# Performance work log

Hardware: AMD Instinct MI355X
Metric: run time of the kernel (lower is better)

## Reference

```python
import math
import jax, jax.numpy as jnp
import numpy as np

D_MODEL = 512
MAX_SEQ = 512
NUM_OUT = 16
H = 1  # num_heads


def _pos_encoding(d_model, seq_len):
    # sinusoidal PE, then flipped along the sequence axis (ReversedPositionalEncoding)
    pos = jnp.arange(seq_len, dtype=jnp.float32)[:, None]
    i = jnp.arange(0, d_model, 2, dtype=jnp.float32)
    ang = pos * jnp.exp(i * (-(math.log(10000.0) / d_model)))  # [S, d/2]
    pe = jnp.stack([jnp.sin(ang), jnp.cos(ang)], axis=-1).reshape(seq_len, d_model)
    return pe[::-1]


def _layernorm(x, w, b, eps=1e-5):
    m = jnp.mean(x, axis=-1, keepdims=True)
    v = jnp.mean(jnp.square(x - m), axis=-1, keepdims=True)
    return (x - m) / jnp.sqrt(v + eps) * w + b


def setup_inputs() -> dict:
    key = jax.random.key(0)
    ks = jax.random.split(key, 8)
    B = 128
    latents = jax.random.normal(ks[0], (B, D_MODEL, MAX_SEQ), dtype=jnp.float32)
    query_mask = jnp.ones((B, NUM_OUT), dtype=jnp.float32)
    query = 0.02 * jax.random.normal(ks[1], (NUM_OUT, D_MODEL), dtype=jnp.float32)
    return {
        "latents": latents,
        "query_mask": query_mask,
        "query": query,
        "ln_lat_w": jnp.ones((D_MODEL,), jnp.float32),
        "ln_lat_b": jnp.zeros((D_MODEL,), jnp.float32),
        "ln_q_w": jnp.ones((D_MODEL,), jnp.float32),
        "ln_q_b": jnp.zeros((D_MODEL,), jnp.float32),
        "Wq": 0.02 * jax.random.normal(ks[2], (D_MODEL, D_MODEL), jnp.float32),
        "bq": jnp.zeros((D_MODEL,), jnp.float32),
        "Wk": 0.02 * jax.random.normal(ks[3], (D_MODEL, D_MODEL), jnp.float32),
        "bk": jnp.zeros((D_MODEL,), jnp.float32),
        "Wv": 0.02 * jax.random.normal(ks[4], (D_MODEL, D_MODEL), jnp.float32),
        "bv": jnp.zeros((D_MODEL,), jnp.float32),
        "Wo": 0.02 * jax.random.normal(ks[5], (1, D_MODEL), jnp.float32),
        "bo": jnp.zeros((1,), jnp.float32),
    }


def reference(latents, query_mask, query, ln_lat_w, ln_lat_b, ln_q_w, ln_q_b,
              Wq, bq, Wk, bk, Wv, bv, Wo, bo):
    B, _, N = latents.shape  # latents: [B, d_model, N]
    scale = math.sqrt(D_MODEL)
    Dh = D_MODEL // H

    # cross-attention mask: query_mask [B,Nq] x all-ones latent mask [B,N]
    mask = jnp.einsum('bq,bk->bqk', query_mask, jnp.ones((B, N), latents.dtype))

    x = jnp.swapaxes(latents, 1, 2) * scale           # [B, N, d]
    x = x + _pos_encoding(D_MODEL, MAX_SEQ)[-N:]      # reversed PE, last N positions
    # dropout is identity in eval mode
    x = _layernorm(x, ln_lat_w, ln_lat_b)

    q = _layernorm(query * scale, ln_q_w, ln_q_b)     # [Nq, d]
    q = jnp.broadcast_to(q[None], (B, NUM_OUT, D_MODEL))

    qh = (q @ Wq.T + bq).reshape(B, NUM_OUT, H, Dh)
    kh = (x @ Wk.T + bk).reshape(B, N, H, Dh)
    vh = (x @ Wv.T + bv).reshape(B, N, H, Dh)

    scores = jnp.einsum('bqhd,bkhd->bhqk', qh, kh) / math.sqrt(Dh)
    scores = jnp.where(mask[:, None] == 0, -1e9, scores)
    attn_weights = jax.nn.softmax(scores, axis=-1)    # [B, H, Nq, N]

    attn = jnp.einsum('bhqk,bkhd->bqhd', attn_weights, vh).reshape(B, NUM_OUT, H * Dh)
    wipe = jnp.all(mask == 0, axis=2, keepdims=True)  # [B, Nq, 1]
    attn = jnp.where(wipe, 0.0, attn)

    logits = attn @ Wo.T + bo                         # [B, Nq, 1]
    return logits, attn_weights
```

## Files before the change

kernel.cpp:

```cpp
#include <hip/hip_runtime.h>
#include <math.h>

#define DM 512
#define NQ 16
#define NG (NQ + 1)
#define NR (NG + 2)

typedef __attribute__((ext_vector_type(2))) float f32x2;

__device__ __forceinline__ float wave_reduce_sum(float v) {
    #pragma unroll
    for (int off = 32; off > 0; off >>= 1) v += __shfl_xor(v, off, 64);
    return v;
}
__device__ __forceinline__ float wave_reduce_max(float v) {
    #pragma unroll
    for (int off = 32; off > 0; off >>= 1) v = fmaxf(v, __shfl_xor(v, off, 64));
    return v;
}

__global__ void k1_setup(const float* __restrict__ Wk, const float* __restrict__ Wv,
                         const float* __restrict__ query,
                         const float* __restrict__ ln_q_w, const float* __restrict__ ln_q_b,
                         float* __restrict__ PET, float* __restrict__ WkT,
                         float* __restrict__ WvT, float* __restrict__ q_ln, int N) {
    __shared__ float tile[64][65];
    int bx = blockIdx.x;
    int lane = threadIdx.x & 63;
    int w = threadIdx.x >> 6;

    if (bx < 128) {
        int ntile = bx & 7, jg = bx >> 3;
        int n = ntile * 64 + lane;
        float p = (float)(N - 1 - n);
        const float c = -logf(10000.f) / (float)DM;
        int jbase = jg * 16 + w * 4;
        #pragma unroll
        for (int u = 0; u < 4; ++u) {
            int j = jbase + u;
            float wj = expf((float)(2 * j) * c);
            float ang = p * wj;
            PET[(size_t)(2 * j) * N + n] = sinf(ang);
            PET[(size_t)(2 * j + 1) * N + n] = cosf(ang);
        }
    } else if (bx < 256) {
        int t = bx - 128;
        const float* W = (t >> 6) ? Wv : Wk;
        float* WT = (t >> 6) ? WvT : WkT;
        int tl = t & 63;
        int te = tl >> 3, td = tl & 7;
        #pragma unroll
        for (int i = 0; i < 16; ++i) {
            int el = w * 16 + i;
            tile[el][lane] = W[(size_t)(te * 64 + el) * DM + td * 64 + lane];
        }
        __syncthreads();
        #pragma unroll
        for (int i = 0; i < 16; ++i) {
            int dl = w * 16 + i;
            WT[(size_t)(td * 64 + dl) * DM + te * 64 + lane] = tile[lane][dl];
        }
    } else {
        const float scale = 22.627416997969522f;
        for (int qi = 0; qi < 4; ++qi) {
            int q = w * 4 + qi;
            float vals[8], s = 0.f, s2 = 0.f;
            #pragma unroll
            for (int i = 0; i < 8; ++i) {
                float x = query[q * DM + i * 64 + lane] * scale;
                vals[i] = x; s += x; s2 += x * x;
            }
            s = wave_reduce_sum(s); s2 = wave_reduce_sum(s2);
            float m = s * (1.f / DM);
            float var = s2 * (1.f / DM) - m * m;
            float rstd = rsqrtf(var + 1e-5f);
            #pragma unroll
            for (int i = 0; i < 8; ++i) {
                int d = i * 64 + lane;
                q_ln[q * DM + d] = (vals[i] - m) * rstd * ln_q_w[d] + ln_q_b[d];
            }
        }
    }
}

__global__ void k2_qh(const float* __restrict__ q_ln, const float* __restrict__ Wq,
                      const float* __restrict__ bq, float* __restrict__ qh) {
    int idx = blockIdx.x * 4 + (threadIdx.x >> 6);
    int lane = threadIdx.x & 63;
    int q = idx >> 9, e = idx & 511;
    const float4* wr = (const float4*)(Wq + (size_t)e * DM);
    const float4* xr = (const float4*)(q_ln + (size_t)q * DM);
    float4 w0 = wr[lane * 2], w1 = wr[lane * 2 + 1];
    float4 x0 = xr[lane * 2], x1 = xr[lane * 2 + 1];
    float s = w0.x * x0.x + w0.y * x0.y + w0.z * x0.z + w0.w * x0.w
            + w1.x * x1.x + w1.y * x1.y + w1.z * x1.z + w1.w * x1.w;
    s = wave_reduce_sum(s);
    if (lane == 0) qh[q * DM + e] = s + bq[e];
}

__global__ void k3_qt(const float* __restrict__ qh, const float* __restrict__ WkT,
                      const float* __restrict__ Wo, const float* __restrict__ WvT,
                      const float* __restrict__ lnw,
                      float* __restrict__ qt, float* __restrict__ A,
                      f32x2* __restrict__ A2, float* __restrict__ wvout) {
    int idx = blockIdx.x * 4 + (threadIdx.x >> 6);
    int lane = threadIdx.x & 63;
    int g = idx >> 9, d = idx & 511;
    const float4* wr;
    const float4* xr;
    if (g < NQ) {
        wr = (const float4*)(WkT + (size_t)d * DM);
        xr = (const float4*)(qh + (size_t)g * DM);
    } else {
        wr = (const float4*)(WvT + (size_t)d * DM);
        xr = (const float4*)Wo;
    }
    float4 w0 = wr[lane * 2], w1 = wr[lane * 2 + 1];
    float4 x0 = xr[lane * 2], x1 = xr[lane * 2 + 1];
    float s = w0.x * x0.x + w0.y * x0.y + w0.z * x0.z + w0.w * x0.w
            + w1.x * x1.x + w1.y * x1.y + w1.z * x1.z + w1.w * x1.w;
    s = wave_reduce_sum(s);
    if (lane == 0) {
        if (g < NQ) qt[g * DM + d] = s;
        else wvout[d] = s;
        float a = s * lnw[d];
        A[g * DM + d] = a;
        f32x2 ap; ap.x = a; ap.y = a;
        A2[g * DM + d] = ap;
    }
}

__global__ void k_consts(const float* __restrict__ A, const float* __restrict__ qt,
                         const float* __restrict__ qh, const float* __restrict__ wv,
                         const float* __restrict__ lnb, const float* __restrict__ bk,
                         const float* __restrict__ Wo, const float* __restrict__ bv,
                         float* __restrict__ consts) {
    int lane = threadIdx.x & 63;
    int w = threadIdx.x >> 6;
    int t = blockIdx.x * 4 + w;
    if (t > NQ) return;
    if (t < NQ) {
        float sa = 0.f, sc = 0.f, qb = 0.f;
        #pragma unroll
        for (int i = 0; i < 8; ++i) {
            int d = i * 64 + lane;
            sa += A[t * DM + d];
            sc = fmaf(qt[t * DM + d], lnb[d], sc);
            qb = fmaf(qh[t * DM + d], bk[d], qb);
        }
        sa = wave_reduce_sum(sa);
        sc = wave_reduce_sum(sc);
        qb = wave_reduce_sum(qb);
        if (lane == 0) { consts[t] = sa; consts[16 + t] = sc + qb; }
    } else {
        float sa = 0.f, cv = 0.f, bvo = 0.f;
        #pragma unroll
        for (int i = 0; i < 8; ++i) {
            int d = i * 64 + lane;
            sa += A[NQ * DM + d];
            cv = fmaf(wv[d], lnb[d], cv);
            bvo = fmaf(Wo[d], bv[d], bvo);
        }
        sa = wave_reduce_sum(sa);
        cv = wave_reduce_sum(cv);
        bvo = wave_reduce_sum(bvo);
        if (lane == 0) { consts[32] = sa; consts[33] = cv + bvo; }
    }
}

__launch_bounds__(256, 4)
__global__ void main2_kernel(const float* __restrict__ latents,
                             const float* __restrict__ PET,
                             const f32x2* __restrict__ A2,
                             float* __restrict__ pbuf, int N) {
    int ntiles = N >> 7;
    int ntile = blockIdx.x % ntiles;
    int dh = blockIdx.x / ntiles;
    int b = blockIdx.y;
    int lane = threadIdx.x & 63;
    int w = threadIdx.x >> 6;
    int n0 = ntile * 128 + lane * 2;

    int d0 = __builtin_amdgcn_readfirstlane(dh * 256 + w * 64);
    const float* latf = latents + (size_t)b * DM * N + (size_t)d0 * N + n0;
    const float* petf = PET + (size_t)d0 * N + n0;
    const float scale = 22.627416997969522f;
    f32x2 sc2; sc2.x = scale; sc2.y = scale;

    f32x2 acc[NG];
    #pragma unroll
    for (int i = 0; i < NG; ++i) { acc[i].x = 0.f; acc[i].y = 0.f; }
    f32x2 S1 = {0.f, 0.f}, S2 = {0.f, 0.f};

    const int U = 4;
    const int NC = 64 / U;
    f32x2 xb[2][U], pb[2][U];
    #pragma unroll
    for (int u = 0; u < U; ++u) {
        xb[0][u] = __builtin_nontemporal_load((const f32x2*)(latf + (size_t)u * N));
        pb[0][u] = *(const f32x2*)(petf + (size_t)u * N);
    }
    for (int c = 0; c < NC; c += 2) {
        #pragma unroll
        for (int u = 0; u < U; ++u) {
            size_t dd = (size_t)((c + 1) * U + u) * N;
            xb[1][u] = __builtin_nontemporal_load((const f32x2*)(latf + dd));
            pb[1][u] = *(const f32x2*)(petf + dd);
        }
        #pragma unroll
        for (int u = 0; u < U; ++u) {
            f32x2 y = xb[0][u] * sc2 + pb[0][u];
            S1 += y; S2 += y * y;
            int d = d0 + c * U + u;
            #pragma unroll
            for (int q = 0; q < NG; ++q)
                acc[q] += A2[(size_t)q * DM + d] * y;
        }
        if (c + 2 < NC) {
            #pragma unroll
            for (int u = 0; u < U; ++u) {
                size_t dd = (size_t)((c + 2) * U + u) * N;
                xb[0][u] = __builtin_nontemporal_load((const f32x2*)(latf + dd));
                pb[0][u] = *(const f32x2*)(petf + dd);
            }
        }
        #pragma unroll
        for (int u = 0; u < U; ++u) {
            f32x2 y = xb[1][u] * sc2 + pb[1][u];
            S1 += y; S2 += y * y;
            int d = d0 + (c + 1) * U + u;
            #pragma unroll
            for (int q = 0; q < NG; ++q)
                acc[q] += A2[(size_t)q * DM + d] * y;
        }
    }

    __shared__ f32x2 red[4][NR][64];
    red[w][0][lane] = S1;
    red[w][1][lane] = S2;
    #pragma unroll
    for (int i = 0; i < NG; ++i) red[w][2 + i][lane] = acc[i];
    __syncthreads();
    if (w != 0) return;

    float* pout = pbuf + (((size_t)dh * gridDim.y + b) * NR) * N + n0;
    #pragma unroll
    for (int i = 0; i < NR; ++i) {
        f32x2 t = red[0][i][lane] + red[1][i][lane] + red[2][i][lane] + red[3][i][lane];
        *(f32x2*)(pout + (size_t)i * N) = t;
    }
}

__global__ void finalize_kernel(const float* __restrict__ pbuf,
                                const float* __restrict__ consts,
                                float* __restrict__ scores,
                                float* __restrict__ vbuf, int N, int B) {
    int t = blockIdx.x * 256 + threadIdx.x;
    int ppb = N >> 1;
    int b = t / ppb;
    int n0 = (t - b * ppb) * 2;
    if (b >= B) return;

    const float* p0 = pbuf + (((size_t)0 * B + b) * NR) * N + n0;
    const float* p1 = pbuf + (((size_t)1 * B + b) * NR) * N + n0;
    f32x2 tot[NR];
    #pragma unroll
    for (int i = 0; i < NR; ++i)
        tot[i] = *(const f32x2*)(p0 + (size_t)i * N) + *(const f32x2*)(p1 + (size_t)i * N);

    f32x2 m = tot[0] * (1.f / DM);
    f32x2 ex2 = tot[1] * (1.f / DM);
    f32x2 rstd;
    rstd.x = rsqrtf(ex2.x - m.x * m.x + 1e-5f);
    rstd.y = rsqrtf(ex2.y - m.y * m.y + 1e-5f);

    float sumAv = consts[32], CvT = consts[33];
    f32x2 v = rstd * (tot[2 + NQ] - m * sumAv) + CvT;
    *(f32x2*)(vbuf + (size_t)b * N + n0) = v;

    const float isd = 0.044194173824159216f;
    #pragma unroll
    for (int q = 0; q < NQ; ++q) {
        f32x2 sc = (rstd * (tot[2 + q] - m * consts[q]) + consts[16 + q]) * isd;
        *(f32x2*)(scores + ((size_t)b * NQ + q) * N + n0) = sc;
    }
}

__global__ void softmax_kernel(const float* __restrict__ scores,
                               const float* __restrict__ vbuf,
                               const float* __restrict__ query_mask,
                               const float* __restrict__ bo,
                               float* __restrict__ out_logits,
                               float* __restrict__ out_attn, int N) {
    int r = blockIdx.x * 4 + (threadIdx.x >> 6);
    int b = r >> 4;
    int lane = threadIdx.x & 63;
    float4* attn_row = (float4*)(out_attn + (size_t)r * N);
    float qm = query_mask[r];
    int nv = N / 4;
    if (qm == 0.f) {
        float u = 1.f / (float)N;
        float4 uv = make_float4(u, u, u, u);
        for (int i = lane; i < nv; i += 64) attn_row[i] = uv;
        if (lane == 0) out_logits[r] = bo[0];
        return;
    }
    const float4* srow = (const float4*)(scores + (size_t)r * N);
    float4 sv[2];
    sv[0] = srow[lane]; sv[1] = srow[64 + lane];
    float mx = fmaxf(fmaxf(fmaxf(sv[0].x, sv[0].y), fmaxf(sv[0].z, sv[0].w)),
                     fmaxf(fmaxf(sv[1].x, sv[1].y), fmaxf(sv[1].z, sv[1].w)));
    mx = wave_reduce_max(mx);
    float sum = 0.f;
    #pragma unroll
    for (int i = 0; i < 2; ++i) {
        sv[i].x = expf(sv[i].x - mx); sv[i].y = expf(sv[i].y - mx);
        sv[i].z = expf(sv[i].z - mx); sv[i].w = expf(sv[i].w - mx);
        sum += sv[i].x + sv[i].y + sv[i].z + sv[i].w;
    }
    sum = wave_reduce_sum(sum);
    float inv = 1.f / sum;
    const float4* vrow = (const float4*)(vbuf + (size_t)b * N);
    float lp = 0.f;
    #pragma unroll
    for (int i = 0; i < 2; ++i) {
        float4 vv = vrow[i * 64 + lane];
        float4 wgt;
        wgt.x = sv[i].x * inv; wgt.y = sv[i].y * inv;
        wgt.z = sv[i].z * inv; wgt.w = sv[i].w * inv;
        attn_row[i * 64 + lane] = wgt;
        lp += wgt.x * vv.x + wgt.y * vv.y + wgt.z * vv.z + wgt.w * vv.w;
    }
    lp = wave_reduce_sum(lp);
    if (lane == 0) out_logits[r] = lp + bo[0];
}

extern "C" void kernel_launch(void* const* d_in, const int* in_sizes, int n_in,
                              void* d_out, int out_size, void* d_ws, size_t ws_size,
                              hipStream_t stream) {
    const float* latents    = (const float*)d_in[0];
    const float* query_mask = (const float*)d_in[1];
    const float* query      = (const float*)d_in[2];
    const float* ln_lat_w   = (const float*)d_in[3];
    const float* ln_lat_b   = (const float*)d_in[4];
    const float* ln_q_w     = (const float*)d_in[5];
    const float* ln_q_b     = (const float*)d_in[6];
    const float* Wq         = (const float*)d_in[7];
    const float* bq         = (const float*)d_in[8];
    const float* Wk         = (const float*)d_in[9];
    const float* bk         = (const float*)d_in[10];
    const float* Wv         = (const float*)d_in[11];
    const float* bv         = (const float*)d_in[12];
    const float* Wo         = (const float*)d_in[13];
    const float* bo         = (const float*)d_in[14];

    int B = in_sizes[1] / NQ;
    int N = in_sizes[0] / (DM * B);

    float* ws = (float*)d_ws;
    size_t off = 0;
    float* PET    = ws + off; off += (size_t)DM * N;
    float* WkT    = ws + off; off += (size_t)DM * DM;
    float* WvT    = ws + off; off += (size_t)DM * DM;
    float* q_ln   = ws + off; off += NQ * DM;
    float* qh     = ws + off; off += NQ * DM;
    float* qt     = ws + off; off += NQ * DM;
    float* A      = ws + off; off += NG * DM;
    float* A2     = ws + off; off += (size_t)NG * DM * 2;
    float* wv     = ws + off; off += DM;
    float* consts = ws + off; off += 64;
    float* scores = ws + off; off += (size_t)B * NQ * N;
    float* vbuf   = ws + off; off += (size_t)B * N;
    float* pbuf   = ws + off; off += (size_t)2 * B * NR * N;

    float* out_logits = (float*)d_out;
    float* out_attn   = out_logits + (size_t)B * NQ;

    k1_setup<<<257, 256, 0, stream>>>(Wk, Wv, query, ln_q_w, ln_q_b,
                                      PET, WkT, WvT, q_ln, N);
    k2_qh<<<NQ * DM / 4, 256, 0, stream>>>(q_ln, Wq, bq, qh);
    k3_qt<<<NG * DM / 4, 256, 0, stream>>>(qh, WkT, Wo, WvT, ln_lat_w,
                                           qt, A, (f32x2*)A2, wv);
    k_consts<<<5, 256, 0, stream>>>(A, qt, qh, wv, ln_lat_b, bk, Wo, bv, consts);
    dim3 gmain((N >> 7) * 2, B);
    main2_kernel<<<gmain, 256, 0, stream>>>(latents, PET, (const f32x2*)A2,
                                            pbuf, N);
    int fin_threads = B * (N / 2);
    finalize_kernel<<<(fin_threads + 255) / 256, 256, 0, stream>>>(
        pbuf, consts, scores, vbuf, N, B);
    softmax_kernel<<<B * NQ / 4, 256, 0, stream>>>(scores, vbuf, query_mask, bo,
                                                   out_logits, out_attn, N);
}
```

Baseline: 245.6 us.

## Fuse query projection into setup, consts into main, finalize with softmax

Merges the query layernorm and Wq projection into the setup kernel, folds the small constants computation into an extra grid row of the main reduction kernel, and combines finalize and softmax into one per-batch kernel that keeps scores and values in shared memory. This removes several kernel launches and the global scores/vbuf round trip. The merged finalize uses one block per batch, which lowers parallelism, and the query layernorm is recomputed redundantly per wave.

```diff
diff --git a/kernel.cpp b/kernel.cpp
--- a/kernel.cpp
+++ b/kernel.cpp
@@ -22,8 +22,9 @@
 __global__ void k1_setup(const float* __restrict__ Wk, const float* __restrict__ Wv,
                          const float* __restrict__ query,
                          const float* __restrict__ ln_q_w, const float* __restrict__ ln_q_b,
+                         const float* __restrict__ Wq, const float* __restrict__ bq,
                          float* __restrict__ PET, float* __restrict__ WkT,
-                         float* __restrict__ WvT, float* __restrict__ q_ln, int N) {
+                         float* __restrict__ WvT, float* __restrict__ qh, int N) {
     __shared__ float tile[64][65];
     int bx = blockIdx.x;
     int lane = threadIdx.x & 63;
@@ -61,41 +62,37 @@
             WT[(size_t)(td * 64 + dl) * DM + te * 64 + lane] = tile[lane][dl];
         }
     } else {
+        int idx = (bx - 256) * 4 + w;
+        int q = idx >> 9, e = idx & 511;
         const float scale = 22.627416997969522f;
-        for (int qi = 0; qi < 4; ++qi) {
-            int q = w * 4 + qi;
-            float vals[8], s = 0.f, s2 = 0.f;
-            #pragma unroll
-            for (int i = 0; i < 8; ++i) {
-                float x = query[q * DM + i * 64 + lane] * scale;
-                vals[i] = x; s += x; s2 += x * x;
-            }
-            s = wave_reduce_sum(s); s2 = wave_reduce_sum(s2);
-            float m = s * (1.f / DM);
-            float var = s2 * (1.f / DM) - m * m;
-            float rstd = rsqrtf(var + 1e-5f);
-            #pragma unroll
-            for (int i = 0; i < 8; ++i) {
-                int d = i * 64 + lane;
-                q_ln[q * DM + d] = (vals[i] - m) * rstd * ln_q_w[d] + ln_q_b[d];
-            }
-        }
-    }
-}
-
-__global__ void k2_qh(const float* __restrict__ q_ln, const float* __restrict__ Wq,
-                      const float* __restrict__ bq, float* __restrict__ qh) {
-    int idx = blockIdx.x * 4 + (threadIdx.x >> 6);
-    int lane = threadIdx.x & 63;
-    int q = idx >> 9, e = idx & 511;
-    const float4* wr = (const float4*)(Wq + (size_t)e * DM);
-    const float4* xr = (const float4*)(q_ln + (size_t)q * DM);
-    float4 w0 = wr[lane * 2], w1 = wr[lane * 2 + 1];
-    float4 x0 = xr[lane * 2], x1 = xr[lane * 2 + 1];
-    float s = w0.x * x0.x + w0.y * x0.y + w0.z * x0.z + w0.w * x0.w
-            + w1.x * x1.x + w1.y * x1.y + w1.z * x1.z + w1.w * x1.w;
-    s = wave_reduce_sum(s);
-    if (lane == 0) qh[q * DM + e] = s + bq[e];
+        const float4* qr = (const float4*)(query + (size_t)q * DM);
+        float4 a0 = qr[lane * 2], a1 = qr[lane * 2 + 1];
+        a0.x *= scale; a0.y *= scale; a0.z *= scale; a0.w *= scale;
+        a1.x *= scale; a1.y *= scale; a1.z *= scale; a1.w *= scale;
+        float s  = a0.x + a0.y + a0.z + a0.w + a1.x + a1.y + a1.z + a1.w;
+        float s2 = a0.x * a0.x + a0.y * a0.y + a0.z * a0.z + a0.w * a0.w
+                 + a1.x * a1.x + a1.y * a1.y + a1.z * a1.z + a1.w * a1.w;
+        s = wave_reduce_sum(s); s2 = wave_reduce_sum(s2);
+        float m = s * (1.f / DM);
+        float var = s2 * (1.f / DM) - m * m;
+        float rstd = rsqrtf(var + 1e-5f);
+        const float4* gw = (const float4*)ln_q_w;
+        const float4* gb = (const float4*)ln_q_b;
+        const float4* wr = (const float4*)(Wq + (size_t)e * DM);
+        float4 w0 = gw[lane * 2], w1 = gw[lane * 2 + 1];
+        float4 b0 = gb[lane * 2], b1 = gb[lane * 2 + 1];
+        float4 W0 = wr[lane * 2], W1 = wr[lane * 2 + 1];
+        float acc = ((a0.x - m) * rstd * w0.x + b0.x) * W0.x
+                  + ((a0.y - m) * rstd * w0.y + b0.y) * W0.y
+                  + ((a0.z - m) * rstd * w0.z + b0.z) * W0.z
+                  + ((a0.w - m) * rstd * w0.w + b0.w) * W0.w
+                  + ((a1.x - m) * rstd * w1.x + b1.x) * W1.x
+                  + ((a1.y - m) * rstd * w1.y + b1.y) * W1.y
+                  + ((a1.z - m) * rstd * w1.z + b1.z) * W1.z
+                  + ((a1.w - m) * rstd * w1.w + b1.w) * W1.w;
+        acc = wave_reduce_sum(acc);
+        if (lane == 0) qh[q * DM + e] = acc + bq[e];
+    }
 }
 
 __global__ void k3_qt(const float* __restrict__ qh, const float* __restrict__ WkT,
@@ -130,55 +127,61 @@
     }
 }
 
-__global__ void k_consts(const float* __restrict__ A, const float* __restrict__ qt,
-                         const float* __restrict__ qh, const float* __restrict__ wv,
-                         const float* __restrict__ lnb, const float* __restrict__ bk,
-                         const float* __restrict__ Wo, const float* __restrict__ bv,
-                         float* __restrict__ consts) {
-    int lane = threadIdx.x & 63;
-    int w = threadIdx.x >> 6;
-    int t = blockIdx.x * 4 + w;
-    if (t > NQ) return;
-    if (t < NQ) {
-        float sa = 0.f, sc = 0.f, qb = 0.f;
-        #pragma unroll
-        for (int i = 0; i < 8; ++i) {
-            int d = i * 64 + lane;
-            sa += A[t * DM + d];
-            sc = fmaf(qt[t * DM + d], lnb[d], sc);
-            qb = fmaf(qh[t * DM + d], bk[d], qb);
-        }
-        sa = wave_reduce_sum(sa);
-        sc = wave_reduce_sum(sc);
-        qb = wave_reduce_sum(qb);
-        if (lane == 0) { consts[t] = sa; consts[16 + t] = sc + qb; }
-    } else {
-        float sa = 0.f, cv = 0.f, bvo = 0.f;
-        #pragma unroll
-        for (int i = 0; i < 8; ++i) {
-            int d = i * 64 + lane;
-            sa += A[NQ * DM + d];
-            cv = fmaf(wv[d], lnb[d], cv);
-            bvo = fmaf(Wo[d], bv[d], bvo);
-        }
-        sa = wave_reduce_sum(sa);
-        cv = wave_reduce_sum(cv);
-        bvo = wave_reduce_sum(bvo);
-        if (lane == 0) { consts[32] = sa; consts[33] = cv + bvo; }
-    }
-}
-
 __launch_bounds__(256, 4)
 __global__ void main2_kernel(const float* __restrict__ latents,
                              const float* __restrict__ PET,
                              const f32x2* __restrict__ A2,
-                             float* __restrict__ pbuf, int N) {
+                             const float* __restrict__ A,
+                             const float* __restrict__ qt,
+                             const float* __restrict__ qh,
+                             const float* __restrict__ wv,
+                             const float* __restrict__ lnb,
+                             const float* __restrict__ bk,
+                             const float* __restrict__ Wo,
+                             const float* __restrict__ bv,
+                             float* __restrict__ pbuf,
+                             float* __restrict__ consts, int N) {
+    int B = gridDim.y - 1;
+    int lane = threadIdx.x & 63;
+    int w = threadIdx.x >> 6;
+    int b = blockIdx.y;
+
+    if (b == B) {
+        int t = blockIdx.x * 4 + w;
+        if (t > NQ) return;
+        if (t < NQ) {
+            float sa = 0.f, sc = 0.f, qb = 0.f;
+            #pragma unroll
+            for (int i = 0; i < 8; ++i) {
+                int d = i * 64 + lane;
+                sa += A[t * DM + d];
+                sc = fmaf(qt[t * DM + d], lnb[d], sc);
+                qb = fmaf(qh[t * DM + d], bk[d], qb);
+            }
+            sa = wave_reduce_sum(sa);
+            sc = wave_reduce_sum(sc);
+            qb = wave_reduce_sum(qb);
+            if (lane == 0) { consts[t] = sa; consts[16 + t] = sc + qb; }
+        } else {
+            float sa = 0.f, cv = 0.f, bvo = 0.f;
+            #pragma unroll
+            for (int i = 0; i < 8; ++i) {
+                int d = i * 64 + lane;
+                sa += A[NQ * DM + d];
+                cv = fmaf(wv[d], lnb[d], cv);
+                bvo = fmaf(Wo[d], bv[d], bvo);
+            }
+            sa = wave_reduce_sum(sa);
+            cv = wave_reduce_sum(cv);
+            bvo = wave_reduce_sum(bvo);
+            if (lane == 0) { consts[32] = sa; consts[33] = cv + bvo; }
+        }
+        return;
+    }
+
     int ntiles = N >> 7;
     int ntile = blockIdx.x % ntiles;
     int dh = blockIdx.x / ntiles;
-    int b = blockIdx.y;
-    int lane = threadIdx.x & 63;
-    int w = threadIdx.x >> 6;
     int n0 = ntile * 128 + lane * 2;
 
     int d0 = __builtin_amdgcn_readfirstlane(dh * 256 + w * 64);
@@ -243,7 +246,7 @@
     __syncthreads();
     if (w != 0) return;
 
-    float* pout = pbuf + (((size_t)dh * gridDim.y + b) * NR) * N + n0;
+    float* pout = pbuf + (((size_t)dh * B + b) * NR) * N + n0;
     #pragma unroll
     for (int i = 0; i < NR; ++i) {
         f32x2 t = red[0][i][lane] + red[1][i][lane] + red[2][i][lane] + red[3][i][lane];
@@ -251,88 +254,85 @@
     }
 }
 
-__global__ void finalize_kernel(const float* __restrict__ pbuf,
-                                const float* __restrict__ consts,
-                                float* __restrict__ scores,
-                                float* __restrict__ vbuf, int N, int B) {
-    int t = blockIdx.x * 256 + threadIdx.x;
-    int ppb = N >> 1;
-    int b = t / ppb;
-    int n0 = (t - b * ppb) * 2;
-    if (b >= B) return;
-
-    const float* p0 = pbuf + (((size_t)0 * B + b) * NR) * N + n0;
-    const float* p1 = pbuf + (((size_t)1 * B + b) * NR) * N + n0;
-    f32x2 tot[NR];
-    #pragma unroll
-    for (int i = 0; i < NR; ++i)
-        tot[i] = *(const f32x2*)(p0 + (size_t)i * N) + *(const f32x2*)(p1 + (size_t)i * N);
-
-    f32x2 m = tot[0] * (1.f / DM);
-    f32x2 ex2 = tot[1] * (1.f / DM);
-    f32x2 rstd;
-    rstd.x = rsqrtf(ex2.x - m.x * m.x + 1e-5f);
-    rstd.y = rsqrtf(ex2.y - m.y * m.y + 1e-5f);
-
-    float sumAv = consts[32], CvT = consts[33];
-    f32x2 v = rstd * (tot[2 + NQ] - m * sumAv) + CvT;
-    *(f32x2*)(vbuf + (size_t)b * N + n0) = v;
-
+__global__ void k_fin(const float* __restrict__ pbuf,
+                      const float* __restrict__ consts,
+                      const float* __restrict__ query_mask,
+                      const float* __restrict__ bo,
+                      float* __restrict__ out_logits,
+                      float* __restrict__ out_attn, int N, int B) {
+    __shared__ float scs[NQ][512];
+    __shared__ float vls[512];
+    int b = blockIdx.x;
+    int tid = threadIdx.x;
     const float isd = 0.044194173824159216f;
-    #pragma unroll
-    for (int q = 0; q < NQ; ++q) {
-        f32x2 sc = (rstd * (tot[2 + q] - m * consts[q]) + consts[16 + q]) * isd;
-        *(f32x2*)(scores + ((size_t)b * NQ + q) * N + n0) = sc;
-    }
-}
-
-__global__ void softmax_kernel(const float* __restrict__ scores,
-                               const float* __restrict__ vbuf,
-                               const float* __restrict__ query_mask,
-                               const float* __restrict__ bo,
-                               float* __restrict__ out_logits,
-                               float* __restrict__ out_attn, int N) {
-    int r = blockIdx.x * 4 + (threadIdx.x >> 6);
-    int b = r >> 4;
-    int lane = threadIdx.x & 63;
-    float4* attn_row = (float4*)(out_attn + (size_t)r * N);
-    float qm = query_mask[r];
-    int nv = N / 4;
-    if (qm == 0.f) {
-        float u = 1.f / (float)N;
-        float4 uv = make_float4(u, u, u, u);
-        for (int i = lane; i < nv; i += 64) attn_row[i] = uv;
-        if (lane == 0) out_logits[r] = bo[0];
-        return;
-    }
-    const float4* srow = (const float4*)(scores + (size_t)r * N);
-    float4 sv[2];
-    sv[0] = srow[lane]; sv[1] = srow[64 + lane];
-    float mx = fmaxf(fmaxf(fmaxf(sv[0].x, sv[0].y), fmaxf(sv[0].z, sv[0].w)),
-                     fmaxf(fmaxf(sv[1].x, sv[1].y), fmaxf(sv[1].z, sv[1].w)));
-    mx = wave_reduce_max(mx);
-    float sum = 0.f;
-    #pragma unroll
-    for (int i = 0; i < 2; ++i) {
-        sv[i].x = expf(sv[i].x - mx); sv[i].y = expf(sv[i].y - mx);
-        sv[i].z = expf(sv[i].z - mx); sv[i].w = expf(sv[i].w - mx);
-        sum += sv[i].x + sv[i].y + sv[i].z + sv[i].w;
-    }
-    sum = wave_reduce_sum(sum);
-    float inv = 1.f / sum;
-    const float4* vrow = (const float4*)(vbuf + (size_t)b * N);
-    float lp = 0.f;
-    #pragma unroll
-    for (int i = 0; i < 2; ++i) {
-        float4 vv = vrow[i * 64 + lane];
-        float4 wgt;
-        wgt.x = sv[i].x * inv; wgt.y = sv[i].y * inv;
-        wgt.z = sv[i].z * inv; wgt.w = sv[i].w * inv;
-        attn_row[i * 64 + lane] = wgt;
-        lp += wgt.x * vv.x + wgt.y * vv.y + wgt.z * vv.z + wgt.w * vv.w;
-    }
-    lp = wave_reduce_sum(lp);
-    if (lane == 0) out_logits[r] = lp + bo[0];
+    float c32 = consts[32], c33 = consts[33];
+
+    for (int np = tid; np < (N >> 1); np += 256) {
+        int n0 = np * 2;
+        const float* p0 = pbuf + (((size_t)0 * B + b) * NR) * N + n0;
+        const float* p1 = pbuf + (((size_t)1 * B + b) * NR) * N + n0;
+        f32x2 tot[NR];
+        #pragma unroll
+        for (int i = 0; i < NR; ++i)
+            tot[i] = *(const f32x2*)(p0 + (size_t)i * N)
+                   + *(const f32x2*)(p1 + (size_t)i * N);
+        f32x2 m = tot[0] * (1.f / DM);
+        f32x2 ex2 = tot[1] * (1.f / DM);
+        f32x2 rstd;
+        rstd.x = rsqrtf(ex2.x - m.x * m.x + 1e-5f);
+        rstd.y = rsqrtf(ex2.y - m.y * m.y + 1e-5f);
+        f32x2 v = rstd * (tot[2 + NQ] - m * c32) + c33;
+        *(f32x2*)&vls[n0] = v;
+        #pragma unroll
+        for (int q = 0; q < NQ; ++q) {
+            f32x2 sc = (rstd * (tot[2 + q] - m * consts[q]) + consts[16 + q]) * isd;
+            *(f32x2*)&scs[q][n0] = sc;
+        }
+    }
+    __syncthreads();
+
+    int lane = tid & 63, w = tid >> 6;
+    int nv = N >> 2;
+    for (int q = w; q < NQ; q += 4) {
+        int r = b * NQ + q;
+        float qm = query_mask[r];
+        float4* arow = (float4*)(out_attn + (size_t)r * N);
+        if (qm == 0.f) {
+            float u = 1.f / (float)N;
+            float4 uv = make_float4(u, u, u, u);
+            for (int i = lane; i < nv; i += 64) arow[i] = uv;
+            if (lane == 0) out_logits[r] = bo[0];
+            continue;
+        }
+        const float4* srow = (const float4*)scs[q];
+        float4 sv[2];
+        sv[0] = srow[lane]; sv[1] = srow[64 + lane];
+        float mx = fmaxf(fmaxf(fmaxf(sv[0].x, sv[0].y), fmaxf(sv[0].z, sv[0].w)),
+                         fmaxf(fmaxf(sv[1].x, sv[1].y), fmaxf(sv[1].z, sv[1].w)));
+        mx = wave_reduce_max(mx);
+        float sum = 0.f;
+        #pragma unroll
+        for (int i = 0; i < 2; ++i) {
+            sv[i].x = expf(sv[i].x - mx); sv[i].y = expf(sv[i].y - mx);
+            sv[i].z = expf(sv[i].z - mx); sv[i].w = expf(sv[i].w - mx);
+            sum += sv[i].x + sv[i].y + sv[i].z + sv[i].w;
+        }
+        sum = wave_reduce_sum(sum);
+        float inv = 1.f / sum;
+        const float4* vrow = (const float4*)vls;
+        float lp = 0.f;
+        #pragma unroll
+        for (int i = 0; i < 2; ++i) {
+            float4 vv = vrow[i * 64 + lane];
+            float4 wgt;
+            wgt.x = sv[i].x * inv; wgt.y = sv[i].y * inv;
+            wgt.z = sv[i].z * inv; wgt.w = sv[i].w * inv;
+            arow[i * 64 + lane] = wgt;
+            lp += wgt.x * vv.x + wgt.y * vv.y + wgt.z * vv.z + wgt.w * vv.w;
+        }
+        lp = wave_reduce_sum(lp);
+        if (lane == 0) out_logits[r] = lp + bo[0];
+    }
 }
 
 extern "C" void kernel_launch(void* const* d_in, const int* in_sizes, int n_in,
@@ -362,32 +362,25 @@
     float* PET    = ws + off; off += (size_t)DM * N;
     float* WkT    = ws + off; off += (size_t)DM * DM;
     float* WvT    = ws + off; off += (size_t)DM * DM;
-    float* q_ln   = ws + off; off += NQ * DM;
     float* qh     = ws + off; off += NQ * DM;
     float* qt     = ws + off; off += NQ * DM;
     float* A      = ws + off; off += NG * DM;
     float* A2     = ws + off; off += (size_t)NG * DM * 2;
     float* wv     = ws + off; off += DM;
     float* consts = ws + off; off += 64;
-    float* scores = ws + off; off += (size_t)B * NQ * N;
-    float* vbuf   = ws + off; off += (size_t)B * N;
     float* pbuf   = ws + off; off += (size_t)2 * B * NR * N;
 
     float* out_logits = (float*)d_out;
     float* out_attn   = out_logits + (size_t)B * NQ;
 
-    k1_setup<<<257, 256, 0, stream>>>(Wk, Wv, query, ln_q_w, ln_q_b,
-                                      PET, WkT, WvT, q_ln, N);
-    k2_qh<<<NQ * DM / 4, 256, 0, stream>>>(q_ln, Wq, bq, qh);
+    k1_setup<<<256 + NQ * DM / 4, 256, 0, stream>>>(
+        Wk, Wv, query, ln_q_w, ln_q_b, Wq, bq, PET, WkT, WvT, qh, N);
     k3_qt<<<NG * DM / 4, 256, 0, stream>>>(qh, WkT, Wo, WvT, ln_lat_w,
                                            qt, A, (f32x2*)A2, wv);
-    k_consts<<<5, 256, 0, stream>>>(A, qt, qh, wv, ln_lat_b, bk, Wo, bv, consts);
-    dim3 gmain((N >> 7) * 2, B);
+    dim3 gmain((N >> 7) * 2, B + 1);
     main2_kernel<<<gmain, 256, 0, stream>>>(latents, PET, (const f32x2*)A2,
-                                            pbuf, N);
-    int fin_threads = B * (N / 2);
-    finalize_kernel<<<(fin_threads + 255) / 256, 256, 0, stream>>>(
-        pbuf, consts, scores, vbuf, N, B);
-    softmax_kernel<<<B * NQ / 4, 256, 0, stream>>>(scores, vbuf, query_mask, bo,
-                                                   out_logits, out_attn, N);
-}
+                                            A, qt, qh, wv, ln_lat_b, bk, Wo, bv,
+                                            pbuf, consts, N);
+    k_fin<<<B, 256, 0, stream>>>(pbuf, consts, query_mask, bo,
+                                 out_logits, out_attn, N, B);
+}
```

New measurement: 240.9 us. No clear change (-1.9%).
